# Optimization experiments

Measured on AMD Instinct MI355X. Metric: run time of the kernel, lower is better.

Reference implementation:

```python
import jax, jax.numpy as jnp
import numpy as np

D_MODEL = 1024
NUM_HEADS = 16
D_K = D_MODEL // NUM_HEADS


def setup_inputs() -> dict:
    key = jax.random.key(0)
    ks = jax.random.split(key, 11)
    B, S = 2, 2048
    scale = 1.0 / np.sqrt(D_MODEL)
    inp = {
        "q": jax.random.normal(ks[0], (B, S, D_MODEL), jnp.float32),
        "k": jax.random.normal(ks[1], (B, S, D_MODEL), jnp.float32),
        "v": jax.random.normal(ks[2], (B, S, D_MODEL), jnp.float32),
        "W_q": jax.random.normal(ks[3], (D_MODEL, D_MODEL), jnp.float32) * scale,
        "b_q": jnp.zeros((D_MODEL,), jnp.float32),
        "W_k": jax.random.normal(ks[4], (D_MODEL, D_MODEL), jnp.float32) * scale,
        "b_k": jnp.zeros((D_MODEL,), jnp.float32),
        "W_v": jax.random.normal(ks[5], (D_MODEL, D_MODEL), jnp.float32) * scale,
        "b_v": jnp.zeros((D_MODEL,), jnp.float32),
        "W_o": jax.random.normal(ks[6], (D_MODEL, D_MODEL), jnp.float32) * scale,
        "b_o": jnp.zeros((D_MODEL,), jnp.float32),
    }
    return inp


def _split_heads(x):
    B, S, _ = x.shape
    return x.reshape(B, S, NUM_HEADS, D_K).transpose(0, 2, 1, 3)  # [B,H,S,Dk]


def reference(q, k, v, W_q, b_q, W_k, b_k, W_v, b_v, W_o, b_o):
    # Linear projections (torch Linear: x @ W.T + b; here W stored as [in,out])
    qh = _split_heads(q @ W_q + b_q)  # [B,H,S,Dk]
    kh = _split_heads(k @ W_k + b_k)
    vh = _split_heads(v @ W_v + b_v)

    scores = jnp.einsum("bhqd,bhkd->bhqk", qh, kh) / jnp.sqrt(
        jnp.asarray(D_K, qh.dtype)
    )  # [B,H,S,S]
    probs = jax.nn.softmax(scores, axis=-1)
    ctx = jnp.einsum("bhqk,bhkd->bhqd", probs, vh)  # [B,H,S,Dk]

    B, H, S, Dk = ctx.shape
    out = ctx.transpose(0, 2, 1, 3).reshape(B, S, D_MODEL)
    return out @ W_o + b_o
```

## Files before the change

### kernel.cpp

```cpp
#include <hip/hip_runtime.h>
#include <stdint.h>

#define DM   1024
#define TOK  4096
#define SEQ  2048
#define NH   16
#define DKH  64
#define WELEM ((size_t)DM * DM)

typedef __bf16 bf16_t;
typedef bf16_t bf16x8 __attribute__((ext_vector_type(8)));
typedef _Float16 f16x8 __attribute__((ext_vector_type(8)));
typedef float  f32x16 __attribute__((ext_vector_type(16)));
typedef uint32_t u32x4 __attribute__((ext_vector_type(4)));

__device__ __forceinline__ uint16_t f2bf(float x) {
  uint32_t u = __builtin_bit_cast(uint32_t, x);
  u += 0x7fffu + ((u >> 16) & 1u);
  return (uint16_t)(u >> 16);
}
__device__ __forceinline__ uint16_t f2h(float x) {
  _Float16 h = (_Float16)x;
  return __builtin_bit_cast(uint16_t, h);
}
__device__ __forceinline__ uint32_t pkrtz(float a, float b) {
  auto h = __builtin_amdgcn_cvt_pkrtz(a, b);
  return __builtin_bit_cast(uint32_t, h);
}
__device__ __forceinline__ bf16x8 ldfrag(const uint16_t* p) {
  uint4 v = *(const uint4*)p;
  return __builtin_bit_cast(bf16x8, v);
}
__device__ __forceinline__ f16x8 ldfragh(const uint16_t* p) {
  uint4 v = *(const uint4*)p;
  return __builtin_bit_cast(f16x8, v);
}
__device__ __forceinline__ uint32_t cvtpk(float lo, float hi) {
  uint32_t r;
  asm("v_cvt_pk_bf16_f32 %0, %1, %2" : "=v"(r) : "v"(lo), "v"(hi));
  return r;
}
__device__ __forceinline__ void plswap(uint32_t& a, uint32_t& b) {
  asm("v_permlane32_swap_b32 %0, %1" : "+v"(a), "+v"(b));
}
__device__ __forceinline__ void gload_lds16(const void* g, void* l) {
  __builtin_amdgcn_global_load_lds(
      (const __attribute__((address_space(1))) uint32_t*)(g),
      (__attribute__((address_space(3))) uint32_t*)(l), 16, 0, 0);
}

__global__ void wsplit_kernel(const float* __restrict__ W0, const float* __restrict__ W1,
                              const float* __restrict__ W2, const float* __restrict__ W3,
                              uint16_t* __restrict__ hi) {
  const float* W = (blockIdx.z == 0) ? W0 : (blockIdx.z == 1) ? W1 : (blockIdx.z == 2) ? W2 : W3;
  uint16_t* hp = hi + blockIdx.z * WELEM;
  __shared__ float t[32][33];
  int n0 = blockIdx.x * 32, k0 = blockIdx.y * 32;
  int tx = threadIdx.x, ty = threadIdx.y;
#pragma unroll
  for (int i = 0; i < 4; i++) {
    int r = ty + i * 8;
    t[r][tx] = W[(size_t)(k0 + r) * DM + n0 + tx];
  }
  __syncthreads();
#pragma unroll
  for (int i = 0; i < 4; i++) {
    int r = ty + i * 8;
    hp[(size_t)(n0 + r) * DM + k0 + tx] = f2h(t[tx][r]);
  }
}

__global__ __launch_bounds__(256, 4) void proj_kernel(
    const float* __restrict__ A0, const float* __restrict__ A1, const float* __restrict__ A2,
    const uint16_t* __restrict__ Whi,
    const float* __restrict__ bA, const float* __restrict__ bB, const float* __restrict__ bC,
    uint16_t* __restrict__ oq, uint16_t* __restrict__ ok, uint16_t* __restrict__ ovt) {
  __shared__ __align__(16) char smem[36864];
  uint16_t* lA  = (uint16_t*)smem;
  uint16_t* lBh = (uint16_t*)(smem + 16384);

  const int tid = threadIdx.x, lane = tid & 63, wid = tid >> 6;
  const int l31 = lane & 31, hi = lane >> 5;
  const int wr = wid >> 1, wc = wid & 1;
  const int bid = blockIdx.x, xcd = bid & 7, idx = bid >> 3;
  const int tm = xcd * 4 + (idx & 3), tn = idx >> 2;

  const int z = (int)blockIdx.y;
  const float* Ap = (z == 0) ? A0 : (z == 1) ? A1 : A2;
  const uint16_t* Bh = Whi + (size_t)z * WELEM;
  const float* bias = (z == 1) ? bB : (z == 2) ? bC : bA;

  f32x16 acc[2][2];
#pragma unroll
  for (int i = 0; i < 2; i++)
#pragma unroll
    for (int j = 0; j < 2; j++)
#pragma unroll
      for (int e = 0; e < 16; e++) acc[i][j][e] = 0.f;

  float4 ar[2][2];

  auto regloadA = [&](int kt) {
#pragma unroll
    for (int p = 0; p < 2; p++) {
      int sid = p * 256 + tid;
      int r = sid >> 2, cs = sid & 3;
      const float* src = Ap + (size_t)(tm * 128 + r) * DM + kt * 32 + cs * 8;
      ar[p][0] = *(const float4*)(src);
      ar[p][1] = *(const float4*)(src + 4);
    }
  };
  auto writeA = [&](int buf) {
#pragma unroll
    for (int p = 0; p < 2; p++) {
      int sid = p * 256 + tid;
      int r = sid >> 2, cs = sid & 3;
      int slot = cs ^ ((r >> 1) & 3);
      u32x4 uu;
      uu[0] = pkrtz(ar[p][0].x, ar[p][0].y);
      uu[1] = pkrtz(ar[p][0].z, ar[p][0].w);
      uu[2] = pkrtz(ar[p][1].x, ar[p][1].y);
      uu[3] = pkrtz(ar[p][1].z, ar[p][1].w);
      *(u32x4*)&lA[buf * 4096 + r * 32 + slot * 8] = uu;
    }
  };
  auto stageB = [&](int buf, int kt) {
#pragma unroll
    for (int p = 0; p < 2; p++) {
      int sid = p * 256 + tid;
      int r = sid >> 2, cs = sid & 3;
      int cg = cs ^ ((r >> 1) & 3);
      size_t offB = (size_t)(tn * 128 + r) * DM + kt * 32 + cg * 8;
      gload_lds16(Bh + offB, &lBh[buf * 4096 + (p * 256 + wid * 64) * 8]);
    }
  };

  regloadA(0);
  stageB(0, 0);
  writeA(0);

  for (int kt = 0; kt < DM / 32; kt++) {
    const int cur = kt & 1;
    __syncthreads();
    if (kt + 1 < DM / 32) {
      regloadA(kt + 1);
      stageB(cur ^ 1, kt + 1);
    }

    f16x8 af[2][2], bh[2][2];
#pragma unroll
    for (int ks = 0; ks < 2; ks++) {
      int cg = ks * 2 + hi;
#pragma unroll
      for (int rt = 0; rt < 2; rt++) {
        int rA = wr * 64 + rt * 32 + l31;
        af[rt][ks] = ldfragh(&lA[cur * 4096 + rA * 32 + (cg ^ ((rA >> 1) & 3)) * 8]);
      }
#pragma unroll
      for (int ct = 0; ct < 2; ct++) {
        int rB = wc * 64 + ct * 32 + l31;
        bh[ct][ks] = ldfragh(&lBh[cur * 4096 + rB * 32 + (cg ^ ((rB >> 1) & 3)) * 8]);
      }
    }
#pragma unroll
    for (int ks = 0; ks < 2; ks++)
#pragma unroll
      for (int rt = 0; rt < 2; rt++)
#pragma unroll
        for (int ct = 0; ct < 2; ct++)
          acc[rt][ct] = __builtin_amdgcn_mfma_f32_32x32x16_f16(af[rt][ks], bh[ct][ks], acc[rt][ct], 0, 0, 0);

    if (kt + 1 < DM / 32) writeA(cur ^ 1);
  }

  if (z == 2) {
    __syncthreads();
    uint16_t* t16 = (uint16_t*)smem;
#pragma unroll
    for (int ct = 0; ct < 2; ct++) {
      int nl = wc * 64 + ct * 32 + l31;
      float bv = bias[tn * 128 + nl];
#pragma unroll
      for (int rt = 0; rt < 2; rt++)
#pragma unroll
        for (int g = 0; g < 16; g++) {
          int ml = wr * 64 + rt * 32 + (g & 3) + 8 * (g >> 2) + 4 * hi;
          t16[nl * 136 + ml] = f2bf(acc[rt][ct][g] + bv);
        }
    }
    __syncthreads();
    int nl2 = tid >> 1, mh = tid & 1;
    int ng = tn * 128 + nl2;
    int hh = ng >> 6, d = ng & 63;
    int b_ = tm >> 4, s0 = (tm & 15) * 128 + mh * 64;
    uint16_t* dst = ovt + (size_t)((b_ * NH + hh) * DKH + d) * SEQ + s0;
    const uint16_t* src = &t16[nl2 * 136 + mh * 64];
#pragma unroll
    for (int j = 0; j < 8; j++)
      ((uint4*)dst)[j] = ((const uint4*)src)[j];
  } else {
#pragma unroll
    for (int ct = 0; ct < 2; ct++) {
      int n = tn * 128 + wc * 64 + ct * 32 + l31;
      float bv = bias[n];
#pragma unroll
      for (int rt = 0; rt < 2; rt++)
#pragma unroll
        for (int g = 0; g < 16; g++) {
          int m = tm * 128 + wr * 64 + rt * 32 + (g & 3) + 8 * (g >> 2) + 4 * hi;
          float val = acc[rt][ct][g] + bv;
          if (z == 0) oq[(size_t)m * DM + n] = f2bf(val * 0.125f);
          else        ok[(size_t)m * DM + n] = f2bf(val);
        }
    }
  }
}

__global__ __launch_bounds__(256, 4) void proj_o_kernel(
    const uint16_t* __restrict__ A, const uint16_t* __restrict__ Bh,
    const float* __restrict__ bias, float* __restrict__ out) {
  __shared__ __attribute__((aligned(16))) uint16_t lA[2][128 * 32];
  __shared__ __attribute__((aligned(16))) uint16_t lBh[2][64 * 32];

  const int tid = threadIdx.x, lane = tid & 63, wid = tid >> 6;
  const int l31 = lane & 31, hi = lane >> 5;
  const int wr = wid >> 1, wc = wid & 1;
  const int bid = blockIdx.x, xcd = bid & 7, idx = bid >> 3;
  const int tm = xcd * 4 + (idx & 3), tn = idx >> 2;

  f32x16 acc[2];
#pragma unroll
  for (int i = 0; i < 2; i++)
#pragma unroll
    for (int e = 0; e < 16; e++) acc[i][e] = 0.f;

  auto stage = [&](int buf, int kt) {
#pragma unroll
    for (int p = 0; p < 2; p++) {
      int sid = p * 256 + tid;
      int r = sid >> 2, cs = sid & 3;
      int cg = cs ^ ((r >> 1) & 3);
      size_t offA = (size_t)(tm * 128 + r) * DM + kt * 32 + cg * 8;
      gload_lds16(A + offA, &lA[buf][(p * 256 + wid * 64) * 8]);
    }
    {
      int r = tid >> 2, cs = tid & 3;
      int cg = cs ^ ((r >> 1) & 3);
      size_t offB = (size_t)(tn * 64 + r) * DM + kt * 32 + cg * 8;
      gload_lds16(Bh + offB, &lBh[buf][wid * 64 * 8]);
    }
  };

  stage(0, 0);
  for (int kt = 0; kt < DM / 32; kt++) {
    const int cur = kt & 1;
    __syncthreads();
    if (kt + 1 < DM / 32) stage(cur ^ 1, kt + 1);

    f16x8 af[2][2], bh[2];
#pragma unroll
    for (int ks = 0; ks < 2; ks++) {
      int cg = ks * 2 + hi;
#pragma unroll
      for (int rt = 0; rt < 2; rt++) {
        int rA = wr * 64 + rt * 32 + l31;
        af[rt][ks] = ldfragh(&lA[cur][rA * 32 + (cg ^ ((rA >> 1) & 3)) * 8]);
      }
      int rB = wc * 32 + l31;
      bh[ks] = ldfragh(&lBh[cur][rB * 32 + (cg ^ ((rB >> 1) & 3)) * 8]);
    }
#pragma unroll
    for (int ks = 0; ks < 2; ks++)
#pragma unroll
      for (int rt = 0; rt < 2; rt++)
        acc[rt] = __builtin_amdgcn_mfma_f32_32x32x16_f16(af[rt][ks], bh[ks], acc[rt], 0, 0, 0);
  }

  const int n = tn * 64 + wc * 32 + l31;
  const float bv = bias[n];
#pragma unroll
  for (int rt = 0; rt < 2; rt++)
#pragma unroll
    for (int g = 0; g < 16; g++) {
      int m = tm * 128 + wr * 64 + rt * 32 + (g & 3) + 8 * (g >> 2) + 4 * hi;
      out[(size_t)m * DM + n] = acc[rt][g] + bv;
    }
}

__global__ __launch_bounds__(256, 2) void attn_kernel(
    const uint16_t* __restrict__ Qp, const uint16_t* __restrict__ Kp,
    const uint16_t* __restrict__ Vt, uint16_t* __restrict__ ctx) {
  __shared__ __align__(16) char smem[65536];
  uint16_t* lK = (uint16_t*)smem;
  uint16_t* lV = (uint16_t*)(smem + 32768);
  const int tid = threadIdx.x, lane = tid & 63, w = tid >> 6;
  const int q31 = lane & 31, hi = lane >> 5;
  const int bid = blockIdx.x, xcd = bid & 7, idx = bid >> 3;
  const int bh_ = xcd * 4 + (idx >> 4), qt = idx & 15;
  const int b = bh_ >> 4, h = bh_ & 15;
  const int bh = bh_;
  const float L2E = 1.44269504089f;
  const float MS = 20.0f * 1.44269504089f;

  auto stage = [&](int buf, int kt) {
#pragma unroll
    for (int p = 0; p < 4; p++) {
      int sid = p * 256 + tid;
      {
        int r = sid >> 3, cs = sid & 7;
        size_t gk = (size_t)(b * SEQ + kt * 128 + r) * DM + h * DKH + (cs ^ (r & 7)) * 8;
        gload_lds16(Kp + gk, lK + buf * 8192 + (p * 256 + w * 64) * 8);
      }
      {
        int r = sid >> 4, cs = sid & 15;
        size_t gv = (size_t)(bh * DKH + r) * SEQ + kt * 128 + (cs ^ (r & 7)) * 8;
        gload_lds16(Vt + gv, lV + buf * 8192 + (p * 256 + w * 64) * 8);
      }
    }
  };

  stage(0, 0);
  bf16x8 qf[4];
  const int qrow = b * SEQ + qt * 128 + w * 32 + q31;
#pragma unroll
  for (int d4 = 0; d4 < 4; d4++)
    qf[d4] = ldfrag(Qp + (size_t)qrow * DM + h * DKH + d4 * 16 + hi * 8);

  f32x16 zz;
#pragma unroll
  for (int i = 0; i < 16; i++) zz[i] = 0.f;
  f32x16 o0 = zz, o1 = zz;
  float l = 0.f;

  for (int kt = 0; kt < SEQ / 128; kt++) {
    const int cur = kt & 1;
    __syncthreads();
    if (kt + 1 < SEQ / 128) stage(cur ^ 1, kt + 1);

    __builtin_amdgcn_s_setprio(1);
    float s0 = 0.f, s1 = 0.f, s2 = 0.f, s3 = 0.f;
#pragma unroll
    for (int kb = 0; kb < 4; kb++) {
      f32x16 a = zz;
#pragma unroll
      for (int d4 = 0; d4 < 4; d4++) {
        int r = kb * 32 + q31;
        int slot = (d4 * 2 + hi) ^ (r & 7);
        bf16x8 kf = ldfrag(lK + cur * 8192 + r * 64 + slot * 8);
        a = __builtin_amdgcn_mfma_f32_32x32x16_bf16(kf, qf[d4], a, 0, 0, 0);
      }
#pragma unroll
      for (int r = 0; r < 16; r += 4) {
        float p0 = __builtin_amdgcn_exp2f(a[r + 0] * L2E - MS);
        float p1 = __builtin_amdgcn_exp2f(a[r + 1] * L2E - MS);
        float p2 = __builtin_amdgcn_exp2f(a[r + 2] * L2E - MS);
        float p3 = __builtin_amdgcn_exp2f(a[r + 3] * L2E - MS);
        a[r + 0] = p0; a[r + 1] = p1;
        a[r + 2] = p2; a[r + 3] = p3;
        s0 += p0; s1 += p1; s2 += p2; s3 += p3;
      }
      uint32_t wv[8];
#pragma unroll
      for (int i = 0; i < 8; i++) wv[i] = cvtpk(a[2 * i], a[2 * i + 1]);
      plswap(wv[0], wv[2]);
      plswap(wv[1], wv[3]);
      plswap(wv[4], wv[6]);
      plswap(wv[5], wv[7]);
      u32x4 c0, c1;
      c0[0] = wv[0]; c0[1] = wv[1]; c0[2] = wv[2]; c0[3] = wv[3];
      c1[0] = wv[4]; c1[1] = wv[5]; c1[2] = wv[6]; c1[3] = wv[7];
      bf16x8 p0f = __builtin_bit_cast(bf16x8, c0);
      bf16x8 p1f = __builtin_bit_cast(bf16x8, c1);
#pragma unroll
      for (int ks = 0; ks < 2; ks++) {
        bf16x8 pa = ks ? p1f : p0f;
        int cg = (kb * 2 + ks) * 2 + hi;
        {
          int r = q31;
          bf16x8 vf = ldfrag(lV + cur * 8192 + r * 128 + (cg ^ (r & 7)) * 8);
          o0 = __builtin_amdgcn_mfma_f32_32x32x16_bf16(vf, pa, o0, 0, 0, 0);
        }
        {
          int r = 32 + q31;
          bf16x8 vf = ldfrag(lV + cur * 8192 + r * 128 + (cg ^ (r & 7)) * 8);
          o1 = __builtin_amdgcn_mfma_f32_32x32x16_bf16(vf, pa, o1, 0, 0, 0);
        }
      }
    }
    __builtin_amdgcn_s_setprio(0);
    l += (s0 + s1) + (s2 + s3);
  }

  l += __shfl_xor(l, 32, 64);
  float rl = 1.f / l;
  __syncthreads();
  uint16_t* th = (uint16_t*)smem;
  int ql = w * 32 + q31;
#pragma unroll
  for (int g4 = 0; g4 < 4; g4++) {
    int d0 = g4 * 8 + hi * 4;
    ushort4 h0, h1;
#pragma unroll
    for (int e = 0; e < 4; e++) {
      ((uint16_t*)&h0)[e] = f2h(o0[g4 * 4 + e] * rl);
      ((uint16_t*)&h1)[e] = f2h(o1[g4 * 4 + e] * rl);
    }
    *(ushort4*)&th[ql * 72 + d0] = h0;
    *(ushort4*)&th[ql * 72 + 32 + d0] = h1;
  }
  __syncthreads();
  int qr = tid >> 1, dh = tid & 1;
  size_t obase = (size_t)(b * SEQ + qt * 128 + qr) * DM + h * DKH + dh * 32;
  const uint16_t* sh = &th[qr * 72 + dh * 32];
#pragma unroll
  for (int j = 0; j < 4; j++)
    ((uint4*)(ctx + obase))[j] = ((const uint4*)sh)[j];
}

extern "C" void kernel_launch(void* const* d_in, const int* in_sizes, int n_in,
                              void* d_out, int out_size, void* d_ws, size_t ws_size,
                              hipStream_t stream) {
  (void)in_sizes; (void)n_in; (void)out_size; (void)ws_size;
  const float* q  = (const float*)d_in[0];
  const float* k  = (const float*)d_in[1];
  const float* v  = (const float*)d_in[2];
  const float* Wq = (const float*)d_in[3];
  const float* bq = (const float*)d_in[4];
  const float* Wk = (const float*)d_in[5];
  const float* bk = (const float*)d_in[6];
  const float* Wv = (const float*)d_in[7];
  const float* bv = (const float*)d_in[8];
  const float* Wo = (const float*)d_in[9];
  const float* bo = (const float*)d_in[10];

  char* ws = (char*)d_ws;
  uint16_t* wt  = (uint16_t*)(ws + ((size_t)0 << 20));
  uint16_t* qp  = (uint16_t*)(ws + ((size_t)8 << 20));
  uint16_t* kp  = (uint16_t*)(ws + ((size_t)16 << 20));
  uint16_t* vt  = (uint16_t*)(ws + ((size_t)24 << 20));
  uint16_t* ctx = (uint16_t*)(ws + ((size_t)32 << 20));

  wsplit_kernel<<<dim3(32, 32, 4), dim3(32, 8), 0, stream>>>(Wq, Wk, Wv, Wo, wt);
  proj_kernel<<<dim3(256, 3), 256, 0, stream>>>(q, k, v, wt,
                                                bq, bk, bv, qp, kp, vt);
  attn_kernel<<<512, 256, 0, stream>>>(qp, kp, vt, ctx);
  proj_o_kernel<<<512, 256, 0, stream>>>(ctx, wt + 3 * WELEM, bo, (float*)d_out);
}
```

Measured before the change: 122.9 us.

## Prefetch A tiles two stages ahead with ping-pong register buffers in QKV GEMM

Restructures the projection GEMM main loop into a 2x-unrolled pipeline with two register buffers for the fp32 A tile. Global loads for A are now issued two k-steps ahead, giving them a full compute stage to land before conversion and the LDS write. This is meant to hide global-load latency for the A operand. It costs extra VGPRs for the second buffer, which may reduce occupancy.

Result: slower. 479.6 us (+290.3%).

```diff
diff --git a/kernel.cpp b/kernel.cpp
--- a/kernel.cpp
+++ b/kernel.cpp
@@ -98,9 +98,9 @@
 #pragma unroll
       for (int e = 0; e < 16; e++) acc[i][j][e] = 0.f;
 
-  float4 ar[2][2];
-
-  auto regloadA = [&](int kt) {
+  float4 arA[2][2], arB[2][2];
+
+  auto regload = [&](float4 (&ar)[2][2], int kt) {
 #pragma unroll
     for (int p = 0; p < 2; p++) {
       int sid = p * 256 + tid;
@@ -110,7 +110,7 @@
       ar[p][1] = *(const float4*)(src + 4);
     }
   };
-  auto writeA = [&](int buf) {
+  auto writeA = [&](const float4 (&ar)[2][2], int buf) {
 #pragma unroll
     for (int p = 0; p < 2; p++) {
       int sid = p * 256 + tid;
@@ -134,19 +134,7 @@
       gload_lds16(Bh + offB, &lBh[buf * 4096 + (p * 256 + wid * 64) * 8]);
     }
   };
-
-  regloadA(0);
-  stageB(0, 0);
-  writeA(0);
-
-  for (int kt = 0; kt < DM / 32; kt++) {
-    const int cur = kt & 1;
-    __syncthreads();
-    if (kt + 1 < DM / 32) {
-      regloadA(kt + 1);
-      stageB(cur ^ 1, kt + 1);
-    }
-
+  auto compute = [&](int buf) {
     f16x8 af[2][2], bh[2][2];
 #pragma unroll
     for (int ks = 0; ks < 2; ks++) {
@@ -154,12 +142,12 @@
 #pragma unroll
       for (int rt = 0; rt < 2; rt++) {
         int rA = wr * 64 + rt * 32 + l31;
-        af[rt][ks] = ldfragh(&lA[cur * 4096 + rA * 32 + (cg ^ ((rA >> 1) & 3)) * 8]);
+        af[rt][ks] = ldfragh(&lA[buf * 4096 + rA * 32 + (cg ^ ((rA >> 1) & 3)) * 8]);
       }
 #pragma unroll
       for (int ct = 0; ct < 2; ct++) {
         int rB = wc * 64 + ct * 32 + l31;
-        bh[ct][ks] = ldfragh(&lBh[cur * 4096 + rB * 32 + (cg ^ ((rB >> 1) & 3)) * 8]);
+        bh[ct][ks] = ldfragh(&lBh[buf * 4096 + rB * 32 + (cg ^ ((rB >> 1) & 3)) * 8]);
       }
     }
 #pragma unroll
@@ -169,8 +157,30 @@
 #pragma unroll
         for (int ct = 0; ct < 2; ct++)
           acc[rt][ct] = __builtin_amdgcn_mfma_f32_32x32x16_f16(af[rt][ks], bh[ct][ks], acc[rt][ct], 0, 0, 0);
-
-    if (kt + 1 < DM / 32) writeA(cur ^ 1);
+  };
+
+  regload(arA, 0);
+  stageB(0, 0);
+  writeA(arA, 0);
+  regload(arB, 1);
+
+  const int NT = DM / 32;
+  for (int kt = 0; kt < NT; kt += 2) {
+    __syncthreads();
+    stageB(1, kt + 1);
+    compute(0);
+    writeA(arB, 1);
+    if (kt + 2 < NT) regload(arA, kt + 2);
+
+    __syncthreads();
+    if (kt + 2 < NT) {
+      stageB(0, kt + 2);
+      compute(1);
+      writeA(arA, 0);
+      if (kt + 3 < NT) regload(arB, kt + 3);
+    } else {
+      compute(1);
+    }
   }
 
   if (z == 2) {
```
